# Performance work log

Measured on AMD Instinct MI355X. Metric: run time of the kernel, lower is better.

Reference implementation:

```python
import jax, jax.numpy as jnp
import numpy as np

PI_OVER_24 = float(np.pi / 24.0)
LN_EPS = 1e-5


def setup_inputs() -> dict:
    key = jax.random.key(0)
    ks = jax.random.split(key, 8)
    B, n, d_model, K = 256, 256, 1024, 2
    return {
        "x_2ch": jax.random.normal(ks[0], (B, n, 2), dtype=jnp.float32),
        "history": jax.random.normal(ks[1], (B, n * 5), dtype=jnp.float32),
        "phi_prev": jax.random.normal(ks[2], (B, K), dtype=jnp.float32),
        "S": jax.random.uniform(ks[3], (n, n), dtype=jnp.float32) * 0.3 + 0.1,
        "W1": jax.random.normal(ks[4], (n * 5, d_model), dtype=jnp.float32) / np.sqrt(n * 5),
        "b1": jnp.zeros((d_model,), dtype=jnp.float32),
        "ln_g": jnp.ones((d_model,), dtype=jnp.float32),
        "ln_b": jnp.zeros((d_model,), dtype=jnp.float32),
        "W2": jax.random.normal(ks[5], (d_model, 2 * K), dtype=jnp.float32) / np.sqrt(d_model),
        "b2": jnp.zeros((2 * K,), dtype=jnp.float32),
        "path_weights": jax.random.normal(ks[6], (n, n, K), dtype=jnp.float32),
    }


def reference(x_2ch, history, phi_prev, S, W1, b1, ln_g, ln_b, W2, b2, path_weights):
    B = x_2ch.shape[0]
    K = path_weights.shape[-1]
    # mode_gen: Linear -> LayerNorm -> ReLU -> Linear
    h = history @ W1 + b1  # [B, d_model]
    mu = jnp.mean(h, axis=-1, keepdims=True)
    var = jnp.mean((h - mu) ** 2, axis=-1, keepdims=True)
    h = (h - mu) * jax.lax.rsqrt(var + LN_EPS) * ln_g + ln_b
    params = (jax.nn.relu(h) @ W2 + b2).reshape(B, K, 2)

    d_phi = jnp.tanh(params[:, :, 0]) * PI_OVER_24  # [B, K]
    phi_curr = phi_prev + d_phi                      # [B, K]
    r_mode = jax.nn.sigmoid(params[:, :, 1])         # [B, K]

    w = jax.nn.softmax(path_weights, axis=-1)        # [n, n, K]
    theta_ij = jnp.einsum('ijk,bk->bij', w, phi_curr)  # [B, n, n]
    r_ij = jnp.einsum('ijk,bk->bij', w, r_mode)        # [B, n, n]

    A_gain = jnp.tanh(r_ij * jax.nn.relu(S)[None]) * 1.1
    cos_t, sin_t = jnp.cos(theta_ij), jnp.sin(theta_ij)
    x_real = x_2ch[:, None, :, 0]  # [B, 1, n]
    x_imag = x_2ch[:, None, :, 1]  # [B, 1, n]
    next_real = jnp.sum(A_gain * (cos_t * x_real - sin_t * x_imag), axis=2)
    next_imag = jnp.sum(A_gain * (sin_t * x_real + cos_t * x_imag), axis=2)
    return jnp.stack([next_real, next_imag], axis=-1), phi_curr, d_phi
```

## Files before the change

### kernel.cpp

```cpp
#include <hip/hip_runtime.h>
#include <math.h>

#define N_   256
#define B_   256
#define DM   1024
#define KH   1280
#define PI24 0.13089969389957473f
#define SPLITS 4
#define KC    320
#define KSUB  64
#define NSUB  5

#define WS_WT   0
#define WS_PART 131072

typedef __attribute__((ext_vector_type(8))) short short8;
typedef __attribute__((ext_vector_type(4))) float f32x4;

__device__ inline unsigned short f2bf(float f) {
    unsigned int u = __float_as_uint(f);
    u += 0x7fffu + ((u >> 16) & 1u);
    return (unsigned short)(u >> 16);
}

__global__ __launch_bounds__(512, 4) void k1_gemm_prep(
    const float* __restrict__ hist, const float* __restrict__ W1,
    const float* __restrict__ pw,   const float* __restrict__ S,
    float* __restrict__ ws) {

    __shared__ union {
        struct {
            unsigned short As[64][72];
            unsigned short Bs[64][72];
        } g;
        float2 ptile[32][33];
    } sh;

    float2* wT = (float2*)(ws + WS_WT);
    float*  Hp = ws + WS_PART;

    int bid = blockIdx.x, tid = threadIdx.x;

    if (bid >= 256) {
        int pb = bid - 256;
        int i0 = (pb >> 3) * 32, j0 = (pb & 7) * 32;
#pragma unroll
        for (int rep = 0; rep < 2; ++rep) {
            int idx = rep * 512 + tid;
            int r = idx >> 5, c = idx & 31;
            float2 p = *(const float2*)&pw[((i0 + r) * N_ + j0 + c) * 2];
            float sv = S[(i0 + r) * N_ + j0 + c];
            float w0 = 1.f / (1.f + __expf(p.y - p.x));
            sh.ptile[r][c] = make_float2(w0, fmaxf(sv, 0.f));
        }
        __syncthreads();
#pragma unroll
        for (int rep = 0; rep < 2; ++rep) {
            int idx = rep * 512 + tid;
            int r = idx >> 5, c = idx & 31;
            wT[(j0 + r) * N_ + i0 + c] = sh.ptile[c][r];
        }
        return;
    }

    int t64 = bid & 63, ksp = bid >> 6;
    int m0 = (t64 >> 4) * 64, n0 = (t64 & 15) * 64;
    int kbase = ksp * KC;

    int lane = tid & 63, wv = tid >> 6;
    int aRow = tid >> 3, aCol = (tid & 7) * 8;
    int bN = tid & 63, bK0 = wv * 8;
    int wrow = wv & 1, wcol = wv >> 1;
    int l16 = lane & 15, lk8 = (lane >> 4) * 8;

    float aRegs[8], bRegs[8];
    {
        const float* ap = &hist[(m0 + aRow) * KH + kbase + aCol];
        *(float4*)&aRegs[0] = *(const float4*)ap;
        *(float4*)&aRegs[4] = *(const float4*)(ap + 4);
#pragma unroll
        for (int i = 0; i < 8; i++)
            bRegs[i] = W1[(kbase + bK0 + i) * DM + n0 + bN];
    }

    f32x4 acc0 = {0.f, 0.f, 0.f, 0.f};
    f32x4 acc1 = {0.f, 0.f, 0.f, 0.f};

    for (int s = 0; s < NSUB; ++s) {
        __syncthreads();
        {
            short8 va, vb;
#pragma unroll
            for (int i = 0; i < 8; i++) {
                va[i] = (short)f2bf(aRegs[i]);
                vb[i] = (short)f2bf(bRegs[i]);
            }
            *(short8*)&sh.g.As[aRow][aCol] = va;
            *(short8*)&sh.g.Bs[bN][bK0] = vb;
        }
        if (s + 1 < NSUB) {
            int kb = kbase + (s + 1) * KSUB;
            const float* ap = &hist[(m0 + aRow) * KH + kb + aCol];
            *(float4*)&aRegs[0] = *(const float4*)ap;
            *(float4*)&aRegs[4] = *(const float4*)(ap + 4);
#pragma unroll
            for (int i = 0; i < 8; i++)
                bRegs[i] = W1[(kb + bK0 + i) * DM + n0 + bN];
        }
        __syncthreads();
#pragma unroll
        for (int ks2 = 0; ks2 < 2; ++ks2) {
            short8 bf = *(const short8*)&sh.g.Bs[wcol * 16 + l16][ks2 * 32 + lk8];
            short8 a0 = *(const short8*)&sh.g.As[wrow * 32 + l16][ks2 * 32 + lk8];
            short8 a1 = *(const short8*)&sh.g.As[wrow * 32 + 16 + l16][ks2 * 32 + lk8];
            acc0 = __builtin_amdgcn_mfma_f32_16x16x32_bf16(a0, bf, acc0, 0, 0, 0);
            acc1 = __builtin_amdgcn_mfma_f32_16x16x32_bf16(a1, bf, acc1, 0, 0, 0);
        }
    }
    {
        float* P = Hp + (size_t)ksp * (B_ * DM);
        int prow = (lane >> 4) * 4;
        int pcol = n0 + wcol * 16 + l16;
#pragma unroll
        for (int r = 0; r < 4; r++) {
            P[(m0 + wrow * 32 + prow + r) * DM + pcol]      = acc0[r];
            P[(m0 + wrow * 32 + 16 + prow + r) * DM + pcol] = acc1[r];
        }
    }
}

__global__ __launch_bounds__(512, 4) void k2_head_main(
    const float* __restrict__ ws_ro, const float* __restrict__ b1,
    const float* __restrict__ lg, const float* __restrict__ lb,
    const float* __restrict__ W2, const float* __restrict__ b2,
    const float* __restrict__ phi_prev, const float* __restrict__ x2,
    float* __restrict__ out) {
    __shared__ float2 hred2[8];
    __shared__ float4 hred4[8];
    __shared__ float  cbc[8];
    __shared__ float2 xs[256];
    __shared__ float2 sred[256];

    const float2* wT = (const float2*)(ws_ro + WS_WT);
    const float*  Hp = ws_ro + WS_PART;

    int b = blockIdx.x;
    int tid = threadIdx.x;
    int lane = tid & 63, wid = tid >> 6;

    ((float*)xs)[tid] = x2[b * (N_ * 2) + tid];

    float2 b12 = *(const float2*)&b1[tid * 2];
    float h0 = b12.x, h1 = b12.y;
#pragma unroll
    for (int s = 0; s < SPLITS; ++s) {
        float2 p = *(const float2*)&Hp[(size_t)s * (B_ * DM) + b * DM + tid * 2];
        h0 += p.x; h1 += p.y;
    }
    float s1v = h0 + h1, s2v = h0 * h0 + h1 * h1;
#pragma unroll
    for (int off = 32; off > 0; off >>= 1) {
        s1v += __shfl_down(s1v, off);
        s2v += __shfl_down(s2v, off);
    }
    if (lane == 0) hred2[wid] = make_float2(s1v, s2v);
    __syncthreads();
    float ms = 0.f, vs = 0.f;
#pragma unroll
    for (int w = 0; w < 8; ++w) { ms += hred2[w].x; vs += hred2[w].y; }
    float mean = ms * (1.f / DM);
    float var  = vs * (1.f / DM) - mean * mean;
    float rstd = rsqrtf(var + 1e-5f);

    float2 g2  = *(const float2*)&lg[tid * 2];
    float2 be2 = *(const float2*)&lb[tid * 2];
    float y0 = fmaxf((h0 - mean) * rstd * g2.x + be2.x, 0.f);
    float y1 = fmaxf((h1 - mean) * rstd * g2.y + be2.y, 0.f);
    float4 wA = *(const float4*)&W2[(tid * 2) * 4];
    float4 wB = *(const float4*)&W2[(tid * 2 + 1) * 4];
    float4 pv;
    pv.x = y0 * wA.x + y1 * wB.x;
    pv.y = y0 * wA.y + y1 * wB.y;
    pv.z = y0 * wA.z + y1 * wB.z;
    pv.w = y0 * wA.w + y1 * wB.w;
#pragma unroll
    for (int off = 32; off > 0; off >>= 1) {
        pv.x += __shfl_down(pv.x, off);
        pv.y += __shfl_down(pv.y, off);
        pv.z += __shfl_down(pv.z, off);
        pv.w += __shfl_down(pv.w, off);
    }
    if (lane == 0) hred4[wid] = pv;
    __syncthreads();
    if (tid == 0) {
        float P0 = b2[0], P1 = b2[1], P2 = b2[2], P3 = b2[3];
#pragma unroll
        for (int w = 0; w < 8; ++w) {
            float4 o = hred4[w];
            P0 += o.x; P1 += o.y; P2 += o.z; P3 += o.w;
        }
        float dphi0 = tanhf(P0) * PI24;
        float dphi1 = tanhf(P2) * PI24;
        float phi0 = phi_prev[b * 2 + 0] + dphi0;
        float phi1 = phi_prev[b * 2 + 1] + dphi1;
        float r0 = 1.f / (1.f + expf(-P1));
        float r1 = 1.f / (1.f + expf(-P3));
        out[B_ * N_ * 2 + b * 2 + 0] = phi0;
        out[B_ * N_ * 2 + b * 2 + 1] = phi1;
        out[B_ * N_ * 2 + B_ * 2 + b * 2 + 0] = dphi0;
        out[B_ * N_ * 2 + B_ * 2 + b * 2 + 1] = dphi1;
        cbc[0] = phi0 - phi1;
        cbc[1] = r1;
        cbc[2] = r0 - r1;
        cbc[3] = cosf(phi1);
        cbc[4] = sinf(phi1);
    }
    __syncthreads();
    float delta = cbc[0], r1v = cbc[1], drv = cbc[2], c1 = cbc[3], sn1 = cbc[4];

    int i = tid & 255, jh = tid >> 8;
    int jbase = jh * 128;
    const float2* wp = &wT[jbase * N_ + i];

    float ar0 = 0.f, ai0 = 0.f, ar1 = 0.f, ai1 = 0.f;
#pragma unroll 4
    for (int jj = 0; jj < 128; jj += 2) {
        {
            float2 w = wp[(size_t)jj * N_];
            float r = fmaf(w.x, drv, r1v);
            float g = r * w.y;
            float u = g * g;
            float tp = fmaf(u, fmaf(u, fmaf(u, -0.059365079f, 0.14666667f),
                                    -0.36666667f), 1.1f);
            float A = g * tp;
            float ang = w.x * delta;
            float sn = __sinf(ang);
            float cs = __cosf(ang);
            float2 xv = xs[jbase + jj];
            float ar = A * cs, as_ = A * sn;
            ar0 = fmaf(ar, xv.x, ar0); ar0 = fmaf(-as_, xv.y, ar0);
            ai0 = fmaf(as_, xv.x, ai0); ai0 = fmaf(ar, xv.y, ai0);
        }
        {
            float2 w = wp[(size_t)(jj + 1) * N_];
            float r = fmaf(w.x, drv, r1v);
            float g = r * w.y;
            float u = g * g;
            float tp = fmaf(u, fmaf(u, fmaf(u, -0.059365079f, 0.14666667f),
                                    -0.36666667f), 1.1f);
            float A = g * tp;
            float ang = w.x * delta;
            float sn = __sinf(ang);
            float cs = __cosf(ang);
            float2 xv = xs[jbase + jj + 1];
            float ar = A * cs, as_ = A * sn;
            ar1 = fmaf(ar, xv.x, ar1); ar1 = fmaf(-as_, xv.y, ar1);
            ai1 = fmaf(as_, xv.x, ai1); ai1 = fmaf(ar, xv.y, ai1);
        }
    }
    float accr = ar0 + ar1, acci = ai0 + ai1;
    if (jh) sred[i] = make_float2(accr, acci);
    __syncthreads();
    if (!jh) {
        float2 o = sred[i];
        accr += o.x; acci += o.y;
        float outr = c1 * accr - sn1 * acci;
        float outi = sn1 * accr + c1 * acci;
        ((float2*)out)[b * N_ + i] = make_float2(outr, outi);
    }
}

extern "C" void kernel_launch(void* const* d_in, const int* in_sizes, int n_in,
                              void* d_out, int out_size, void* d_ws, size_t ws_size,
                              hipStream_t stream) {
    const float* x_2ch    = (const float*)d_in[0];
    const float* history  = (const float*)d_in[1];
    const float* phi_prev = (const float*)d_in[2];
    const float* S        = (const float*)d_in[3];
    const float* W1       = (const float*)d_in[4];
    const float* b1       = (const float*)d_in[5];
    const float* ln_g     = (const float*)d_in[6];
    const float* ln_b     = (const float*)d_in[7];
    const float* W2       = (const float*)d_in[8];
    const float* b2       = (const float*)d_in[9];
    const float* path_w   = (const float*)d_in[10];

    float* out = (float*)d_out;
    float* ws  = (float*)d_ws;

    k1_gemm_prep<<<320, 512, 0, stream>>>(history, W1, path_w, S, ws);
    k2_head_main<<<256, 512, 0, stream>>>(ws, b1, ln_g, ln_b, W2, b2,
                                          phi_prev, x_2ch, out);
}
```

Measured before the change: 27.49 us.

## Pre-convert GEMM operands to bf16 in a separate kernel and drop LDS staging

Adds a conversion kernel that casts history to bf16 and transposes W1 into a K-contiguous bf16 layout, alongside the existing path-weight prep. The GEMM kernel then loads MFMA fragments straight from global memory, with no shared-memory staging or barriers. Split-K is reduced from 4 to 2, so there are fewer partial sums to reduce. The cost is an extra kernel launch and an extra write-then-read round trip of the converted operands, and the GEMM now runs on fewer blocks (128), each with a longer K loop.

```diff
diff --git a/kernel.cpp b/kernel.cpp
--- a/kernel.cpp
+++ b/kernel.cpp
@@ -6,13 +6,13 @@
 #define DM   1024
 #define KH   1280
 #define PI24 0.13089969389957473f
-#define SPLITS 4
-#define KC    320
-#define KSUB  64
-#define NSUB  5
-
-#define WS_WT   0
-#define WS_PART 131072
+#define SPLITS 2
+#define KC    640
+
+#define WS_WT    0
+#define WS_PART  131072
+#define WS_HISTB 655360
+#define WS_W1T   819200
 
 typedef __attribute__((ext_vector_type(8))) short short8;
 typedef __attribute__((ext_vector_type(4))) float f32x4;
@@ -23,26 +23,48 @@
     return (unsigned short)(u >> 16);
 }
 
-__global__ __launch_bounds__(512, 4) void k1_gemm_prep(
+__global__ __launch_bounds__(512, 4) void k0_convert(
     const float* __restrict__ hist, const float* __restrict__ W1,
     const float* __restrict__ pw,   const float* __restrict__ S,
     float* __restrict__ ws) {
-
     __shared__ union {
-        struct {
-            unsigned short As[64][72];
-            unsigned short Bs[64][72];
-        } g;
+        float  t64[64][65];
         float2 ptile[32][33];
     } sh;
 
-    float2* wT = (float2*)(ws + WS_WT);
-    float*  Hp = ws + WS_PART;
+    unsigned short* histB = (unsigned short*)(ws + WS_HISTB);
+    unsigned short* W1T   = (unsigned short*)(ws + WS_W1T);
+    float2*         wT    = (float2*)(ws + WS_WT);
 
     int bid = blockIdx.x, tid = threadIdx.x;
 
-    if (bid >= 256) {
-        int pb = bid - 256;
+    if (bid < 80) {
+        int idx = bid * 4096 + tid * 8;
+        float4 v0 = *(const float4*)&hist[idx];
+        float4 v1 = *(const float4*)&hist[idx + 4];
+        float v[8] = {v0.x, v0.y, v0.z, v0.w, v1.x, v1.y, v1.z, v1.w};
+        short8 o;
+#pragma unroll
+        for (int e = 0; e < 8; e++) o[e] = (short)f2bf(v[e]);
+        *(short8*)&histB[idx] = o;
+    } else if (bid < 400) {
+        int tb = bid - 80;
+        int k0t = (tb >> 4) * 64, n0t = (tb & 15) * 64;
+#pragma unroll
+        for (int rep = 0; rep < 2; ++rep) {
+            int r = rep * 32 + (tid >> 4), c = (tid & 15) * 4;
+            float4 v = *(const float4*)&W1[(k0t + r) * DM + n0t + c];
+            sh.t64[r][c] = v.x; sh.t64[r][c + 1] = v.y;
+            sh.t64[r][c + 2] = v.z; sh.t64[r][c + 3] = v.w;
+        }
+        __syncthreads();
+        int rr = tid >> 3, cc = (tid & 7) * 8;
+        short8 o;
+#pragma unroll
+        for (int j = 0; j < 8; j++) o[j] = (short)f2bf(sh.t64[cc + j][rr]);
+        *(short8*)&W1T[(n0t + rr) * KH + k0t + cc] = o;
+    } else {
+        int pb = bid - 400;
         int i0 = (pb >> 3) * 32, j0 = (pb & 7) * 32;
 #pragma unroll
         for (int rep = 0; rep < 2; ++rep) {
@@ -60,62 +82,37 @@
             int r = idx >> 5, c = idx & 31;
             wT[(j0 + r) * N_ + i0 + c] = sh.ptile[c][r];
         }
-        return;
-    }
-
+    }
+}
+
+__global__ __launch_bounds__(512, 4) void k1_gemm(
+    const float* __restrict__ ws_ro, float* __restrict__ ws) {
+    const unsigned short* histB = (const unsigned short*)(ws_ro + WS_HISTB);
+    const unsigned short* W1T   = (const unsigned short*)(ws_ro + WS_W1T);
+    float* Hp = ws + WS_PART;
+
+    int bid = blockIdx.x, tid = threadIdx.x;
     int t64 = bid & 63, ksp = bid >> 6;
     int m0 = (t64 >> 4) * 64, n0 = (t64 & 15) * 64;
     int kbase = ksp * KC;
 
     int lane = tid & 63, wv = tid >> 6;
-    int aRow = tid >> 3, aCol = (tid & 7) * 8;
-    int bN = tid & 63, bK0 = wv * 8;
     int wrow = wv & 1, wcol = wv >> 1;
     int l16 = lane & 15, lk8 = (lane >> 4) * 8;
 
-    float aRegs[8], bRegs[8];
-    {
-        const float* ap = &hist[(m0 + aRow) * KH + kbase + aCol];
-        *(float4*)&aRegs[0] = *(const float4*)ap;
-        *(float4*)&aRegs[4] = *(const float4*)(ap + 4);
-#pragma unroll
-        for (int i = 0; i < 8; i++)
-            bRegs[i] = W1[(kbase + bK0 + i) * DM + n0 + bN];
-    }
+    const unsigned short* aP = &histB[(m0 + wrow * 32 + l16) * KH + kbase + lk8];
+    const unsigned short* bP = &W1T[(n0 + wcol * 16 + l16) * KH + kbase + lk8];
 
     f32x4 acc0 = {0.f, 0.f, 0.f, 0.f};
     f32x4 acc1 = {0.f, 0.f, 0.f, 0.f};
 
-    for (int s = 0; s < NSUB; ++s) {
-        __syncthreads();
-        {
-            short8 va, vb;
-#pragma unroll
-            for (int i = 0; i < 8; i++) {
-                va[i] = (short)f2bf(aRegs[i]);
-                vb[i] = (short)f2bf(bRegs[i]);
-            }
-            *(short8*)&sh.g.As[aRow][aCol] = va;
-            *(short8*)&sh.g.Bs[bN][bK0] = vb;
-        }
-        if (s + 1 < NSUB) {
-            int kb = kbase + (s + 1) * KSUB;
-            const float* ap = &hist[(m0 + aRow) * KH + kb + aCol];
-            *(float4*)&aRegs[0] = *(const float4*)ap;
-            *(float4*)&aRegs[4] = *(const float4*)(ap + 4);
-#pragma unroll
-            for (int i = 0; i < 8; i++)
-                bRegs[i] = W1[(kb + bK0 + i) * DM + n0 + bN];
-        }
-        __syncthreads();
-#pragma unroll
-        for (int ks2 = 0; ks2 < 2; ++ks2) {
-            short8 bf = *(const short8*)&sh.g.Bs[wcol * 16 + l16][ks2 * 32 + lk8];
-            short8 a0 = *(const short8*)&sh.g.As[wrow * 32 + l16][ks2 * 32 + lk8];
-            short8 a1 = *(const short8*)&sh.g.As[wrow * 32 + 16 + l16][ks2 * 32 + lk8];
-            acc0 = __builtin_amdgcn_mfma_f32_16x16x32_bf16(a0, bf, acc0, 0, 0, 0);
-            acc1 = __builtin_amdgcn_mfma_f32_16x16x32_bf16(a1, bf, acc1, 0, 0, 0);
-        }
+#pragma unroll 4
+    for (int k = 0; k < KC; k += 32) {
+        short8 a0 = *(const short8*)(aP + k);
+        short8 a1 = *(const short8*)(aP + k + 16 * KH);
+        short8 bf = *(const short8*)(bP + k);
+        acc0 = __builtin_amdgcn_mfma_f32_16x16x32_bf16(a0, bf, acc0, 0, 0, 0);
+        acc1 = __builtin_amdgcn_mfma_f32_16x16x32_bf16(a1, bf, acc1, 0, 0, 0);
     }
     {
         float* P = Hp + (size_t)ksp * (B_ * DM);
@@ -288,7 +285,8 @@
     float* out = (float*)d_out;
     float* ws  = (float*)d_ws;
 
-    k1_gemm_prep<<<320, 512, 0, stream>>>(history, W1, path_w, S, ws);
+    k0_convert  <<<464, 512, 0, stream>>>(history, W1, path_w, S, ws);
+    k1_gemm     <<<128, 512, 0, stream>>>(ws, ws);
     k2_head_main<<<256, 512, 0, stream>>>(ws, b1, ln_g, ln_b, W2, b2,
                                           phi_prev, x_2ch, out);
 }
```

Result: slower. 41.37 us (+50.5%).

## Process two batches per block in head kernel, split j across blocks with atomics

Applied to the files above, without the earlier changes.

The head kernel now uses 1024-thread blocks that each handle a pair of batch rows and half of the j range. Each weight load is reused for two batches, and partial sums are combined through shared memory and then atomicAdd into a zeroed output. The price is redundant LayerNorm and head work, since each batch is computed by two blocks, plus an extra memset launch and atomic traffic. The bf16 conversion in the GEMM switches to the HIP intrinsic.

```diff
diff --git a/kernel.cpp b/kernel.cpp
--- a/kernel.cpp
+++ b/kernel.cpp
@@ -1,4 +1,5 @@
 #include <hip/hip_runtime.h>
+#include <hip/hip_bf16.h>
 #include <math.h>
 
 #define N_   256
@@ -8,19 +9,17 @@
 #define PI24 0.13089969389957473f
 #define SPLITS 4
 #define KC    320
-#define KSUB  64
 #define NSUB  5
 
-#define WS_WT   0
-#define WS_PART 131072
+#define WS_WT    0
+#define WS_PART  131072
 
 typedef __attribute__((ext_vector_type(8))) short short8;
 typedef __attribute__((ext_vector_type(4))) float f32x4;
 
-__device__ inline unsigned short f2bf(float f) {
-    unsigned int u = __float_as_uint(f);
-    u += 0x7fffu + ((u >> 16) & 1u);
-    return (unsigned short)(u >> 16);
+__device__ inline short f2bf_s(float f) {
+    __hip_bfloat16 h = __float2bfloat16(f);
+    return *reinterpret_cast<short*>(&h);
 }
 
 __global__ __launch_bounds__(512, 4) void k1_gemm_prep(
@@ -68,19 +67,19 @@
     int kbase = ksp * KC;
 
     int lane = tid & 63, wv = tid >> 6;
+    int wrow = wv & 1, wcol = wv >> 1;
+    int l16 = lane & 15, lk8 = (lane >> 4) * 8;
     int aRow = tid >> 3, aCol = (tid & 7) * 8;
     int bN = tid & 63, bK0 = wv * 8;
-    int wrow = wv & 1, wcol = wv >> 1;
-    int l16 = lane & 15, lk8 = (lane >> 4) * 8;
-
-    float aRegs[8], bRegs[8];
+
+    float4 aV0, aV1; float bV[8];
     {
         const float* ap = &hist[(m0 + aRow) * KH + kbase + aCol];
-        *(float4*)&aRegs[0] = *(const float4*)ap;
-        *(float4*)&aRegs[4] = *(const float4*)(ap + 4);
+        aV0 = *(const float4*)ap;
+        aV1 = *(const float4*)(ap + 4);
 #pragma unroll
         for (int i = 0; i < 8; i++)
-            bRegs[i] = W1[(kbase + bK0 + i) * DM + n0 + bN];
+            bV[i] = W1[(kbase + bK0 + i) * DM + n0 + bN];
     }
 
     f32x4 acc0 = {0.f, 0.f, 0.f, 0.f};
@@ -89,23 +88,21 @@
     for (int s = 0; s < NSUB; ++s) {
         __syncthreads();
         {
+            float av[8] = {aV0.x, aV0.y, aV0.z, aV0.w, aV1.x, aV1.y, aV1.z, aV1.w};
             short8 va, vb;
 #pragma unroll
-            for (int i = 0; i < 8; i++) {
-                va[i] = (short)f2bf(aRegs[i]);
-                vb[i] = (short)f2bf(bRegs[i]);
-            }
+            for (int i = 0; i < 8; i++) { va[i] = f2bf_s(av[i]); vb[i] = f2bf_s(bV[i]); }
             *(short8*)&sh.g.As[aRow][aCol] = va;
             *(short8*)&sh.g.Bs[bN][bK0] = vb;
         }
         if (s + 1 < NSUB) {
-            int kb = kbase + (s + 1) * KSUB;
+            int kb = kbase + (s + 1) * 64;
             const float* ap = &hist[(m0 + aRow) * KH + kb + aCol];
-            *(float4*)&aRegs[0] = *(const float4*)ap;
-            *(float4*)&aRegs[4] = *(const float4*)(ap + 4);
+            aV0 = *(const float4*)ap;
+            aV1 = *(const float4*)(ap + 4);
 #pragma unroll
             for (int i = 0; i < 8; i++)
-                bRegs[i] = W1[(kb + bK0 + i) * DM + n0 + bN];
+                bV[i] = W1[(kb + bK0 + i) * DM + n0 + bN];
         }
         __syncthreads();
 #pragma unroll
@@ -129,32 +126,38 @@
     }
 }
 
-__global__ __launch_bounds__(512, 4) void k2_head_main(
+__global__ __launch_bounds__(1024, 1) void k2_head_main(
     const float* __restrict__ ws_ro, const float* __restrict__ b1,
     const float* __restrict__ lg, const float* __restrict__ lb,
     const float* __restrict__ W2, const float* __restrict__ b2,
     const float* __restrict__ phi_prev, const float* __restrict__ x2,
     float* __restrict__ out) {
-    __shared__ float2 hred2[8];
-    __shared__ float4 hred4[8];
-    __shared__ float  cbc[8];
-    __shared__ float2 xs[256];
-    __shared__ float2 sred[256];
+    __shared__ float2 hred2[16];
+    __shared__ float4 hred4[16];
+    __shared__ float  cbc[2][8];
+    __shared__ float2 xs[2][128];
+    __shared__ float4 sred[3][256];
 
     const float2* wT = (const float2*)(ws_ro + WS_WT);
     const float*  Hp = ws_ro + WS_PART;
 
-    int b = blockIdx.x;
-    int tid = threadIdx.x;
+    int bid = blockIdx.x, tid = threadIdx.x;
+    int b0 = (bid >> 1) * 2;
+    int jhb = bid & 1;
     int lane = tid & 63, wid = tid >> 6;
-
-    ((float*)xs)[tid] = x2[b * (N_ * 2) + tid];
-
-    float2 b12 = *(const float2*)&b1[tid * 2];
+    int t = tid & 511, bh = tid >> 9;
+    int b = b0 + bh;
+
+    if (tid < 512) {
+        int bx = tid >> 8, jj = tid & 255;
+        ((float*)&xs[bx][0])[jj] = x2[(b0 + bx) * (N_ * 2) + jhb * 256 + jj];
+    }
+
+    float2 b12 = *(const float2*)&b1[t * 2];
     float h0 = b12.x, h1 = b12.y;
 #pragma unroll
     for (int s = 0; s < SPLITS; ++s) {
-        float2 p = *(const float2*)&Hp[(size_t)s * (B_ * DM) + b * DM + tid * 2];
+        float2 p = *(const float2*)&Hp[(size_t)s * (B_ * DM) + b * DM + t * 2];
         h0 += p.x; h1 += p.y;
     }
     float s1v = h0 + h1, s2v = h0 * h0 + h1 * h1;
@@ -167,17 +170,17 @@
     __syncthreads();
     float ms = 0.f, vs = 0.f;
 #pragma unroll
-    for (int w = 0; w < 8; ++w) { ms += hred2[w].x; vs += hred2[w].y; }
+    for (int w = 0; w < 8; ++w) { ms += hred2[bh * 8 + w].x; vs += hred2[bh * 8 + w].y; }
     float mean = ms * (1.f / DM);
     float var  = vs * (1.f / DM) - mean * mean;
     float rstd = rsqrtf(var + 1e-5f);
 
-    float2 g2  = *(const float2*)&lg[tid * 2];
-    float2 be2 = *(const float2*)&lb[tid * 2];
+    float2 g2  = *(const float2*)&lg[t * 2];
+    float2 be2 = *(const float2*)&lb[t * 2];
     float y0 = fmaxf((h0 - mean) * rstd * g2.x + be2.x, 0.f);
     float y1 = fmaxf((h1 - mean) * rstd * g2.y + be2.y, 0.f);
-    float4 wA = *(const float4*)&W2[(tid * 2) * 4];
-    float4 wB = *(const float4*)&W2[(tid * 2 + 1) * 4];
+    float4 wA = *(const float4*)&W2[(t * 2) * 4];
+    float4 wB = *(const float4*)&W2[(t * 2 + 1) * 4];
     float4 pv;
     pv.x = y0 * wA.x + y1 * wB.x;
     pv.y = y0 * wA.y + y1 * wB.y;
@@ -192,11 +195,11 @@
     }
     if (lane == 0) hred4[wid] = pv;
     __syncthreads();
-    if (tid == 0) {
+    if (t == 0) {
         float P0 = b2[0], P1 = b2[1], P2 = b2[2], P3 = b2[3];
 #pragma unroll
         for (int w = 0; w < 8; ++w) {
-            float4 o = hred4[w];
+            float4 o = hred4[bh * 8 + w];
             P0 += o.x; P1 += o.y; P2 += o.z; P3 += o.w;
         }
         float dphi0 = tanhf(P0) * PI24;
@@ -209,66 +212,78 @@
         out[B_ * N_ * 2 + b * 2 + 1] = phi1;
         out[B_ * N_ * 2 + B_ * 2 + b * 2 + 0] = dphi0;
         out[B_ * N_ * 2 + B_ * 2 + b * 2 + 1] = dphi1;
-        cbc[0] = phi0 - phi1;
-        cbc[1] = r1;
-        cbc[2] = r0 - r1;
-        cbc[3] = cosf(phi1);
-        cbc[4] = sinf(phi1);
+        cbc[bh][0] = phi0 - phi1;
+        cbc[bh][1] = r1;
+        cbc[bh][2] = r0 - r1;
+        cbc[bh][3] = cosf(phi1);
+        cbc[bh][4] = sinf(phi1);
     }
     __syncthreads();
-    float delta = cbc[0], r1v = cbc[1], drv = cbc[2], c1 = cbc[3], sn1 = cbc[4];
-
-    int i = tid & 255, jh = tid >> 8;
-    int jbase = jh * 128;
-    const float2* wp = &wT[jbase * N_ + i];
+    float dl0 = cbc[0][0], r10 = cbc[0][1], dr0 = cbc[0][2];
+    float dl1 = cbc[1][0], r11 = cbc[1][1], dr1 = cbc[1][2];
+
+    int i = tid & 255, jq = tid >> 8;
+    int jloc = jq * 32;
+    const float2* wp = &wT[(jhb * 128 + jloc) * N_ + i];
 
     float ar0 = 0.f, ai0 = 0.f, ar1 = 0.f, ai1 = 0.f;
 #pragma unroll 4
-    for (int jj = 0; jj < 128; jj += 2) {
+    for (int jj = 0; jj < 32; ++jj) {
+        float2 w = wp[(size_t)jj * N_];
+        float u_base;
+        float2 xv0 = xs[0][jloc + jj];
+        float2 xv1 = xs[1][jloc + jj];
         {
-            float2 w = wp[(size_t)jj * N_];
-            float r = fmaf(w.x, drv, r1v);
+            float r = fmaf(w.x, dr0, r10);
             float g = r * w.y;
             float u = g * g;
             float tp = fmaf(u, fmaf(u, fmaf(u, -0.059365079f, 0.14666667f),
                                     -0.36666667f), 1.1f);
             float A = g * tp;
-            float ang = w.x * delta;
+            float ang = w.x * dl0;
             float sn = __sinf(ang);
             float cs = __cosf(ang);
-            float2 xv = xs[jbase + jj];
             float ar = A * cs, as_ = A * sn;
-            ar0 = fmaf(ar, xv.x, ar0); ar0 = fmaf(-as_, xv.y, ar0);
-            ai0 = fmaf(as_, xv.x, ai0); ai0 = fmaf(ar, xv.y, ai0);
+            ar0 = fmaf(ar, xv0.x, ar0); ar0 = fmaf(-as_, xv0.y, ar0);
+            ai0 = fmaf(as_, xv0.x, ai0); ai0 = fmaf(ar, xv0.y, ai0);
         }
         {
-            float2 w = wp[(size_t)(jj + 1) * N_];
-            float r = fmaf(w.x, drv, r1v);
+            float r = fmaf(w.x, dr1, r11);
             float g = r * w.y;
             float u = g * g;
             float tp = fmaf(u, fmaf(u, fmaf(u, -0.059365079f, 0.14666667f),
                                     -0.36666667f), 1.1f);
             float A = g * tp;
-            float ang = w.x * delta;
+            float ang = w.x * dl1;
             float sn = __sinf(ang);
             float cs = __cosf(ang);
-            float2 xv = xs[jbase + jj + 1];
             float ar = A * cs, as_ = A * sn;
-            ar1 = fmaf(ar, xv.x, ar1); ar1 = fmaf(-as_, xv.y, ar1);
-            ai1 = fmaf(as_, xv.x, ai1); ai1 = fmaf(ar, xv.y, ai1);
-        }
-    }
-    float accr = ar0 + ar1, acci = ai0 + ai1;
-    if (jh) sred[i] = make_float2(accr, acci);
+            ar1 = fmaf(ar, xv1.x, ar1); ar1 = fmaf(-as_, xv1.y, ar1);
+            ai1 = fmaf(as_, xv1.x, ai1); ai1 = fmaf(ar, xv1.y, ai1);
+        }
+        (void)u_base;
+    }
+    if (jq) sred[jq - 1][i] = make_float4(ar0, ai0, ar1, ai1);
     __syncthreads();
-    if (!jh) {
-        float2 o = sred[i];
-        accr += o.x; acci += o.y;
-        float outr = c1 * accr - sn1 * acci;
-        float outi = sn1 * accr + c1 * acci;
-        ((float2*)out)[b * N_ + i] = make_float2(outr, outi);
+    if (!jq) {
+#pragma unroll
+        for (int q = 0; q < 3; ++q) {
+            float4 o = sred[q][i];
+            ar0 += o.x; ai0 += o.y; ar1 += o.z; ai1 += o.w;
+        }
+        float c10 = cbc[0][3], s10 = cbc[0][4];
+        float c11 = cbc[1][3], s11 = cbc[1][4];
+        float o0r = c10 * ar0 - s10 * ai0;
+        float o0i = s10 * ar0 + c10 * ai0;
+        float o1r = c11 * ar1 - s11 * ai1;
+        float o1i = s11 * ar1 + c11 * ai1;
+        atomicAdd(&out[(b0 * N_ + i) * 2],     o0r);
+        atomicAdd(&out[(b0 * N_ + i) * 2 + 1], o0i);
+        atomicAdd(&out[((b0 + 1) * N_ + i) * 2],     o1r);
+        atomicAdd(&out[((b0 + 1) * N_ + i) * 2 + 1], o1i);
     }
 }
+
 
 extern "C" void kernel_launch(void* const* d_in, const int* in_sizes, int n_in,
                               void* d_out, int out_size, void* d_ws, size_t ws_size,
@@ -288,7 +303,9 @@
     float* out = (float*)d_out;
     float* ws  = (float*)d_ws;
 
+    hipMemsetAsync(out, 0, (size_t)B_ * N_ * 2 * sizeof(float), stream);
+
     k1_gemm_prep<<<320, 512, 0, stream>>>(history, W1, path_w, S, ws);
-    k2_head_main<<<256, 512, 0, stream>>>(ws, b1, ln_g, ln_b, W2, b2,
-                                          phi_prev, x_2ch, out);
+    k2_head_main<<<256, 1024, 0, stream>>>(ws, b1, ln_g, ln_b, W2, b2,
+                                           phi_prev, x_2ch, out);
 }
```

Result: slower. 33.22 us (+20.9%).
